# Kernel optimization log

Measured on AMD Instinct MI355X. Metric: run time of the kernel, lower is better.

Reference implementation:

```python
import jax, jax.numpy as jnp
import numpy as np

B, S, D, H = 4, 1024, 1024, 16
DK = D // H
EPS = 1e-6


def setup_inputs() -> dict:
    key = jax.random.key(0)
    ks = jax.random.split(key, 12)
    s = 1.0 / np.sqrt(D)
    inp = {
        "query": jax.random.normal(ks[0], (B, S, D), jnp.float32),
        "key": jax.random.normal(ks[1], (B, S, D), jnp.float32),
        "value": jax.random.normal(ks[2], (B, S, D), jnp.float32),
        "Wq": jax.random.normal(ks[3], (D, D), jnp.float32) * s,
        "bq": jnp.zeros((D,), jnp.float32),
        "Wk": jax.random.normal(ks[4], (D, D), jnp.float32) * s,
        "bk": jnp.zeros((D,), jnp.float32),
        "Wv": jax.random.normal(ks[5], (D, D), jnp.float32) * s,
        "bv": jnp.zeros((D,), jnp.float32),
        "Wo": jax.random.normal(ks[6], (D, D), jnp.float32) * s,
        "bo": jnp.zeros((D,), jnp.float32),
        "gamma": jnp.ones((D,), jnp.float32),
        "beta": jnp.zeros((D,), jnp.float32),
    }
    return inp


def reference(query, key, value, Wq, bq, Wk, bk, Wv, bv, Wo, bo, gamma, beta):
    residual = query
    # QKV projections, split into heads: [B,S,D] -> [B,H,S,DK]
    q = (query @ Wq + bq).reshape(B, S, H, DK).transpose(0, 2, 1, 3)
    k = (key @ Wk + bk).reshape(B, S, H, DK).transpose(0, 2, 1, 3)
    v = (value @ Wv + bv).reshape(B, S, H, DK).transpose(0, 2, 1, 3)
    # scaled dot-product attention (dropout is identity in eval mode)
    scores = jnp.einsum("bhqd,bhkd->bhqk", q, k) / jnp.sqrt(jnp.float32(DK))
    attn = jax.nn.softmax(scores, axis=-1)  # [B,H,S,S]
    x = jnp.einsum("bhqk,bhkd->bhqd", attn, v)
    x = x.transpose(0, 2, 1, 3).reshape(B, S, D)
    # residual + LayerNorm(eps=1e-6)
    x = x + residual
    mu = jnp.mean(x, axis=-1, keepdims=True)
    var = jnp.mean(jnp.square(x - mu), axis=-1, keepdims=True)
    x = (x - mu) * jax.lax.rsqrt(var + EPS) * gamma + beta
    out = x @ Wo + bo
    return (out, attn)
```

## Files before the change

### kernel.cpp

```cpp
#include <hip/hip_runtime.h>

typedef unsigned short u16;
typedef __attribute__((ext_vector_type(8))) short bf16x8;
typedef __attribute__((ext_vector_type(4))) float f32x4;

struct __align__(8) us4 { u16 x, y, z, w; };

#define B_  4
#define S_  1024
#define D_  1024
#define H_  16
#define DK_ 64

__device__ __forceinline__ u16 f2bf(float x) {
    union { float f; unsigned int u; } c; c.f = x;
    unsigned int r = (c.u + 0x7FFFu + ((c.u >> 16) & 1u)) >> 16;
    return (u16)r;
}

__device__ __forceinline__ void gload_lds16(const void* g, void* l) {
    __builtin_amdgcn_global_load_lds(
        (const __attribute__((address_space(1))) unsigned int*)g,
        (__attribute__((address_space(3))) unsigned int*)l, 16, 0, 0);
}

__global__ __launch_bounds__(256) void cvt_x(const float* __restrict__ q,
                                             const float* __restrict__ k,
                                             const float* __restrict__ v,
                                             u16* __restrict__ xq,
                                             u16* __restrict__ xk,
                                             u16* __restrict__ xv) {
    const float* src = (blockIdx.y == 0) ? q : (blockIdx.y == 1) ? k : v;
    u16* dst        = (blockIdx.y == 0) ? xq : (blockIdx.y == 1) ? xk : xv;
    int idx = (blockIdx.x * 256 + threadIdx.x) * 4;
    f32x4 f = *(const f32x4*)(src + idx);
    us4 o; o.x = f2bf(f[0]); o.y = f2bf(f[1]); o.z = f2bf(f[2]); o.w = f2bf(f[3]);
    *(us4*)(dst + idx) = o;
}

__global__ __launch_bounds__(256) void cvt_w(const float* __restrict__ w0, const float* __restrict__ w1,
                                             const float* __restrict__ w2, const float* __restrict__ w3,
                                             u16* __restrict__ t0, u16* __restrict__ t1,
                                             u16* __restrict__ t2, u16* __restrict__ t3) {
    __shared__ float t[64][65];
    const float* W = (blockIdx.z == 0) ? w0 : (blockIdx.z == 1) ? w1 : (blockIdx.z == 2) ? w2 : w3;
    u16* T        = (blockIdx.z == 0) ? t0 : (blockIdx.z == 1) ? t1 : (blockIdx.z == 2) ? t2 : t3;
    int k0 = blockIdx.x * 64, n0 = blockIdx.y * 64;
    int tid = threadIdx.x;
    int r4 = tid >> 6, c = tid & 63;
#pragma unroll
    for (int i = 0; i < 16; i++) {
        int r = i * 4 + r4;
        t[r][c] = W[(size_t)(k0 + r) * 1024 + n0 + c];
    }
    __syncthreads();
#pragma unroll
    for (int i = 0; i < 16; i++) {
        int r = i * 4 + r4;
        T[(size_t)(n0 + r) * 1024 + k0 + c] = f2bf(t[c][r]);
    }
}

__device__ __forceinline__ void gemm_core(const u16* __restrict__ X, const u16* __restrict__ WT,
                                          const float* __restrict__ bias, void* __restrict__ outp,
                                          int mode, float scale, int bm, int bn) {
    __shared__ u16 Al[128 * 32];
    __shared__ u16 Bl[128 * 32];
    int tid = threadIdx.x, l = tid & 63, w = tid >> 6;
    int lr = l & 15, lq = l >> 4;
    int wm = (w >> 1) * 64, wn = (w & 1) * 64;
    f32x4 acc[4][4] = {};
    for (int kk = 0; kk < 1024; kk += 32) {
        __syncthreads();
#pragma unroll
        for (int i = 0; i < 2; i++) {
            int flat = tid * 16 + i * 4096;
            int row = flat >> 6, kb = flat & 63;
            gload_lds16((const char*)X + ((size_t)(bm * 128 + row) * 2048 + (size_t)kk * 2 + kb),
                        (char*)Al + flat);
            gload_lds16((const char*)WT + ((size_t)(bn * 128 + row) * 2048 + (size_t)kk * 2 + kb),
                        (char*)Bl + flat);
        }
        asm volatile("s_waitcnt vmcnt(0)" ::: "memory");
        __syncthreads();
        bf16x8 af[4], bfr[4];
#pragma unroll
        for (int ms = 0; ms < 4; ms++)
            af[ms] = *(const bf16x8*)(Al + (wm + ms * 16 + lr) * 32 + lq * 8);
#pragma unroll
        for (int ns = 0; ns < 4; ns++)
            bfr[ns] = *(const bf16x8*)(Bl + (wn + ns * 16 + lr) * 32 + lq * 8);
#pragma unroll
        for (int ms = 0; ms < 4; ms++)
#pragma unroll
            for (int ns = 0; ns < 4; ns++)
                acc[ms][ns] = __builtin_amdgcn_mfma_f32_16x16x32_bf16(af[ms], bfr[ns], acc[ms][ns], 0, 0, 0);
    }
#pragma unroll
    for (int ns = 0; ns < 4; ns++) {
        int n = bn * 128 + wn + ns * 16 + lr;
        float bv_ = bias[n];
#pragma unroll
        for (int ms = 0; ms < 4; ms++) {
            int mbase = bm * 128 + wm + ms * 16 + lq * 4;
            if (mode == 0) {
                u16* o = (u16*)outp;
                int h = n >> 6, dk = n & 63;
#pragma unroll
                for (int r = 0; r < 4; r++) {
                    int m = mbase + r;
                    int b = m >> 10, s = m & 1023;
                    o[((size_t)(b * H_ + h) * 1024 + s) * 64 + dk] = f2bf((acc[ms][ns][r] + bv_) * scale);
                }
            } else if (mode == 1) {
                u16* o = (u16*)outp;
                int h = n >> 6, dk = n & 63;
                int b = mbase >> 10, s0 = mbase & 1023;
                us4 pk;
                pk.x = f2bf(acc[ms][ns][0] + bv_);
                pk.y = f2bf(acc[ms][ns][1] + bv_);
                pk.z = f2bf(acc[ms][ns][2] + bv_);
                pk.w = f2bf(acc[ms][ns][3] + bv_);
                *(us4*)(o + ((size_t)(b * H_ + h) * 64 + dk) * 1024 + s0) = pk;
            } else {
                float* o = (float*)outp;
#pragma unroll
                for (int r = 0; r < 4; r++) {
                    int m = mbase + r;
                    o[(size_t)m * 1024 + n] = acc[ms][ns][r] + bv_;
                }
            }
        }
    }
}

__global__ __launch_bounds__(256) void gemm_qkv(const u16* __restrict__ Xq, const u16* __restrict__ Xk,
                                                const u16* __restrict__ Xv,
                                                const u16* __restrict__ Wq, const u16* __restrict__ Wk,
                                                const u16* __restrict__ Wv,
                                                const float* __restrict__ bq, const float* __restrict__ bk,
                                                const float* __restrict__ bv,
                                                u16* __restrict__ Qh, u16* __restrict__ Kh,
                                                u16* __restrict__ VT) {
    int z = blockIdx.z;
    const u16* X = (z == 0) ? Xq : (z == 1) ? Xk : Xv;
    const u16* W = (z == 0) ? Wq : (z == 1) ? Wk : Wv;
    const float* bia = (z == 0) ? bq : (z == 1) ? bk : bv;
    void* out = (z == 0) ? (void*)Qh : (z == 1) ? (void*)Kh : (void*)VT;
    int mode = (z == 2) ? 1 : 0;
    float scale = (z == 0) ? 0.125f : 1.0f;
    gemm_core(X, W, bia, out, mode, scale, blockIdx.x, blockIdx.y);
}

__global__ __launch_bounds__(256) void gemm_out(const u16* __restrict__ X, const u16* __restrict__ WT,
                                                const float* __restrict__ bias, float* __restrict__ outp) {
    gemm_core(X, WT, bias, outp, 2, 1.0f, blockIdx.x, blockIdx.y);
}

__global__ __launch_bounds__(256) void attn_fused(const u16* __restrict__ Qh, const u16* __restrict__ Kh,
                                                  const u16* __restrict__ VT,
                                                  float* __restrict__ attn_out, float* __restrict__ x_out) {
    __shared__ u16 P_lds[4][4096];
    __shared__ float red[4][16][64];
    __shared__ float redm[4][16];
    __shared__ float reds[4][16];
    int tid = threadIdx.x, l = tid & 63, w = tid >> 6;
    int lr = l & 15, lq = l >> 4;
    int q0 = blockIdx.x * 16, bh = blockIdx.y;
    const u16* qp = Qh + (size_t)bh * 65536;
    const u16* kp = Kh + (size_t)bh * 65536;
    const u16* vp = VT + (size_t)bh * 65536;

    bf16x8 aq0 = *(const bf16x8*)(qp + (q0 + lr) * 64 + lq * 8);
    bf16x8 aq1 = *(const bf16x8*)(qp + (q0 + lr) * 64 + 32 + lq * 8);

    f32x4 sc[16];
#pragma unroll
    for (int n = 0; n < 16; n++) {
        int kb = w * 256 + n * 16;
        bf16x8 b0 = *(const bf16x8*)(kp + (size_t)(kb + lr) * 64 + lq * 8);
        bf16x8 b1 = *(const bf16x8*)(kp + (size_t)(kb + lr) * 64 + 32 + lq * 8);
        f32x4 a = {};
        a = __builtin_amdgcn_mfma_f32_16x16x32_bf16(aq0, b0, a, 0, 0, 0);
        a = __builtin_amdgcn_mfma_f32_16x16x32_bf16(aq1, b1, a, 0, 0, 0);
        sc[n] = a;
    }

#pragma unroll
    for (int r = 0; r < 4; r++) {
        float m = sc[0][r];
#pragma unroll
        for (int n = 1; n < 16; n++) m = fmaxf(m, sc[n][r]);
#pragma unroll
        for (int off = 1; off < 16; off <<= 1) m = fmaxf(m, __shfl_xor(m, off));
        if (lr == 0) redm[w][lq * 4 + r] = m;
    }
    __syncthreads();
    float inv[4];
#pragma unroll
    for (int r = 0; r < 4; r++) {
        int row = lq * 4 + r;
        float M = fmaxf(fmaxf(redm[0][row], redm[1][row]), fmaxf(redm[2][row], redm[3][row]));
        float s = 0.f;
#pragma unroll
        for (int n = 0; n < 16; n++) {
            float p = __expf(sc[n][r] - M);
            sc[n][r] = p;
            s += p;
        }
#pragma unroll
        for (int off = 1; off < 16; off <<= 1) s += __shfl_xor(s, off);
        if (lr == 0) reds[w][row] = s;
    }
    __syncthreads();
#pragma unroll
    for (int r = 0; r < 4; r++) {
        int row = lq * 4 + r;
        inv[r] = 1.0f / (reds[0][row] + reds[1][row] + reds[2][row] + reds[3][row]);
    }

    size_t abase = (size_t)bh * 1048576 + (size_t)q0 * 1024 + w * 256;
#pragma unroll
    for (int n = 0; n < 16; n++) {
#pragma unroll
        for (int r = 0; r < 4; r++) {
            float p = sc[n][r] * inv[r];
            attn_out[abase + (size_t)(lq * 4 + r) * 1024 + n * 16 + lr] = p;
            int row = lq * 4 + r, col = n * 16 + lr;
            P_lds[w][row * 256 + (col ^ ((row & 3) << 4))] = f2bf(p);
        }
    }
    __syncthreads();

    f32x4 pv[4] = {};
#pragma unroll
    for (int kk = 0; kk < 8; kk++) {
        int col = kk * 32 + lq * 8;
        bf16x8 ap = *(const bf16x8*)(&P_lds[w][lr * 256 + (col ^ ((lr & 3) << 4))]);
#pragma unroll
        for (int ns = 0; ns < 4; ns++) {
            bf16x8 bv_ = *(const bf16x8*)(vp + (size_t)(ns * 16 + lr) * 1024 + w * 256 + kk * 32 + lq * 8);
            pv[ns] = __builtin_amdgcn_mfma_f32_16x16x32_bf16(ap, bv_, pv[ns], 0, 0, 0);
        }
    }
#pragma unroll
    for (int ns = 0; ns < 4; ns++)
#pragma unroll
        for (int r = 0; r < 4; r++)
            red[w][lq * 4 + r][ns * 16 + lr] = pv[ns][r];
    __syncthreads();

    int qq = tid >> 4, dk = (tid & 15) * 4;
    f32x4 acc = *(const f32x4*)&red[0][qq][dk];
#pragma unroll
    for (int w2 = 1; w2 < 4; w2++) acc += *(const f32x4*)&red[w2][qq][dk];
    int b = bh >> 4, h = bh & 15;
    *(f32x4*)(x_out + ((size_t)(b * 1024 + q0 + qq)) * 1024 + h * 64 + dk) = acc;
}

__global__ __launch_bounds__(256) void ln_kernel(const float* __restrict__ x, const float* __restrict__ resid,
                                                 const float* __restrict__ gamma, const float* __restrict__ beta,
                                                 u16* __restrict__ out) {
    int row = blockIdx.x, tid = threadIdx.x;
    int l = tid & 63, w = tid >> 6;
    size_t base = (size_t)row * 1024 + tid * 4;
    f32x4 v = *(const f32x4*)(x + base);
    f32x4 rz = *(const f32x4*)(resid + base);
    v += rz;
    float s = v[0] + v[1] + v[2] + v[3];
    float s2 = v[0] * v[0] + v[1] * v[1] + v[2] * v[2] + v[3] * v[3];
#pragma unroll
    for (int off = 1; off < 64; off <<= 1) {
        s += __shfl_xor(s, off);
        s2 += __shfl_xor(s2, off);
    }
    __shared__ float as_[4], as2_[4];
    if (l == 0) { as_[w] = s; as2_[w] = s2; }
    __syncthreads();
    s = as_[0] + as_[1] + as_[2] + as_[3];
    s2 = as2_[0] + as2_[1] + as2_[2] + as2_[3];
    float mean = s * (1.f / 1024.f);
    float var = s2 * (1.f / 1024.f) - mean * mean;
    float rs = rsqrtf(var + 1e-6f);
    f32x4 g = *(const f32x4*)(gamma + tid * 4);
    f32x4 bt = *(const f32x4*)(beta + tid * 4);
    us4 o;
    o.x = f2bf((v[0] - mean) * rs * g[0] + bt[0]);
    o.y = f2bf((v[1] - mean) * rs * g[1] + bt[1]);
    o.z = f2bf((v[2] - mean) * rs * g[2] + bt[2]);
    o.w = f2bf((v[3] - mean) * rs * g[3] + bt[3]);
    *(us4*)(out + base) = o;
}

extern "C" void kernel_launch(void* const* d_in, const int* in_sizes, int n_in,
                              void* d_out, int out_size, void* d_ws, size_t ws_size,
                              hipStream_t stream) {
    const float* query = (const float*)d_in[0];
    const float* key   = (const float*)d_in[1];
    const float* value = (const float*)d_in[2];
    const float* Wq    = (const float*)d_in[3];
    const float* bq    = (const float*)d_in[4];
    const float* Wk    = (const float*)d_in[5];
    const float* bk    = (const float*)d_in[6];
    const float* Wv    = (const float*)d_in[7];
    const float* bv    = (const float*)d_in[8];
    const float* Wo    = (const float*)d_in[9];
    const float* bo    = (const float*)d_in[10];
    const float* gamma = (const float*)d_in[11];
    const float* beta  = (const float*)d_in[12];

    char* ws = (char*)d_ws;
    u16* XQ  = (u16*)(ws + 0);
    u16* XK  = (u16*)(ws + 8388608);
    u16* XV  = (u16*)(ws + 16777216);
    u16* WQT = (u16*)(ws + 25165824);
    u16* WKT = (u16*)(ws + 27262976);
    u16* WVT = (u16*)(ws + 29360128);
    u16* WOT = (u16*)(ws + 31457280);
    u16* Qh  = (u16*)(ws + 33554432);
    u16* Kh  = (u16*)(ws + 41943040);
    u16* VT  = (u16*)(ws + 50331648);
    float* PV = (float*)(ws + 0);
    u16* LN  = (u16*)(ws + 16777216);

    float* outp = (float*)d_out;
    float* attn = outp + 4194304;

    cvt_x<<<dim3(4096, 3), 256, 0, stream>>>(query, key, value, XQ, XK, XV);
    cvt_w<<<dim3(16, 16, 4), 256, 0, stream>>>(Wq, Wk, Wv, Wo, WQT, WKT, WVT, WOT);
    gemm_qkv<<<dim3(32, 8, 3), 256, 0, stream>>>(XQ, XK, XV, WQT, WKT, WVT, bq, bk, bv, Qh, Kh, VT);
    attn_fused<<<dim3(64, 64), 256, 0, stream>>>(Qh, Kh, VT, attn, PV);
    ln_kernel<<<4096, 256, 0, stream>>>(PV, query, gamma, beta, LN);
    gemm_out<<<dim3(32, 8), 256, 0, stream>>>(LN, WOT, bo, outp);
}
```

Before: 249.3 us.

## Deepen GEMM K-tile, narrow output GEMM tile, and remap attention blocks per XCD

```diff
diff --git a/kernel.cpp b/kernel.cpp
--- a/kernel.cpp
+++ b/kernel.cpp
@@ -61,49 +61,59 @@
     }
 }
 
+template <int BN, int MODE>
 __device__ __forceinline__ void gemm_core(const u16* __restrict__ X, const u16* __restrict__ WT,
                                           const float* __restrict__ bias, void* __restrict__ outp,
-                                          int mode, float scale, int bm, int bn) {
-    __shared__ u16 Al[128 * 32];
-    __shared__ u16 Bl[128 * 32];
+                                          float scale, int bm, int bn) {
+    constexpr int NS = BN / 32;
+    __shared__ u16 Al[128 * 64];
+    __shared__ u16 Bl[BN * 64];
     int tid = threadIdx.x, l = tid & 63, w = tid >> 6;
     int lr = l & 15, lq = l >> 4;
-    int wm = (w >> 1) * 64, wn = (w & 1) * 64;
-    f32x4 acc[4][4] = {};
-    for (int kk = 0; kk < 1024; kk += 32) {
+    int wm = (w >> 1) * 64, wn = (w & 1) * (BN / 2);
+    f32x4 acc[4][NS] = {};
+    for (int kk = 0; kk < 1024; kk += 64) {
         __syncthreads();
 #pragma unroll
-        for (int i = 0; i < 2; i++) {
+        for (int i = 0; i < 4; i++) {
             int flat = tid * 16 + i * 4096;
-            int row = flat >> 6, kb = flat & 63;
+            int row = flat >> 7, kb = flat & 127;
             gload_lds16((const char*)X + ((size_t)(bm * 128 + row) * 2048 + (size_t)kk * 2 + kb),
                         (char*)Al + flat);
-            gload_lds16((const char*)WT + ((size_t)(bn * 128 + row) * 2048 + (size_t)kk * 2 + kb),
+        }
+#pragma unroll
+        for (int i = 0; i < BN / 32; i++) {
+            int flat = tid * 16 + i * 4096;
+            int row = flat >> 7, kb = flat & 127;
+            gload_lds16((const char*)WT + ((size_t)(bn * BN + row) * 2048 + (size_t)kk * 2 + kb),
                         (char*)Bl + flat);
         }
         asm volatile("s_waitcnt vmcnt(0)" ::: "memory");
         __syncthreads();
-        bf16x8 af[4], bfr[4];
-#pragma unroll
-        for (int ms = 0; ms < 4; ms++)
-            af[ms] = *(const bf16x8*)(Al + (wm + ms * 16 + lr) * 32 + lq * 8);
-#pragma unroll
-        for (int ns = 0; ns < 4; ns++)
-            bfr[ns] = *(const bf16x8*)(Bl + (wn + ns * 16 + lr) * 32 + lq * 8);
-#pragma unroll
-        for (int ms = 0; ms < 4; ms++)
-#pragma unroll
-            for (int ns = 0; ns < 4; ns++)
-                acc[ms][ns] = __builtin_amdgcn_mfma_f32_16x16x32_bf16(af[ms], bfr[ns], acc[ms][ns], 0, 0, 0);
-    }
-#pragma unroll
-    for (int ns = 0; ns < 4; ns++) {
-        int n = bn * 128 + wn + ns * 16 + lr;
+#pragma unroll
+        for (int kkk = 0; kkk < 2; kkk++) {
+            bf16x8 af[4], bfr[NS];
+#pragma unroll
+            for (int ms = 0; ms < 4; ms++)
+                af[ms] = *(const bf16x8*)(Al + (wm + ms * 16 + lr) * 64 + kkk * 32 + lq * 8);
+#pragma unroll
+            for (int ns = 0; ns < NS; ns++)
+                bfr[ns] = *(const bf16x8*)(Bl + (wn + ns * 16 + lr) * 64 + kkk * 32 + lq * 8);
+#pragma unroll
+            for (int ms = 0; ms < 4; ms++)
+#pragma unroll
+                for (int ns = 0; ns < NS; ns++)
+                    acc[ms][ns] = __builtin_amdgcn_mfma_f32_16x16x32_bf16(af[ms], bfr[ns], acc[ms][ns], 0, 0, 0);
+        }
+    }
+#pragma unroll
+    for (int ns = 0; ns < NS; ns++) {
+        int n = bn * BN + wn + ns * 16 + lr;
         float bv_ = bias[n];
 #pragma unroll
         for (int ms = 0; ms < 4; ms++) {
             int mbase = bm * 128 + wm + ms * 16 + lq * 4;
-            if (mode == 0) {
+            if (MODE == 0) {
                 u16* o = (u16*)outp;
                 int h = n >> 6, dk = n & 63;
 #pragma unroll
@@ -112,7 +122,7 @@
                     int b = m >> 10, s = m & 1023;
                     o[((size_t)(b * H_ + h) * 1024 + s) * 64 + dk] = f2bf((acc[ms][ns][r] + bv_) * scale);
                 }
-            } else if (mode == 1) {
+            } else if (MODE == 1) {
                 u16* o = (u16*)outp;
                 int h = n >> 6, dk = n & 63;
                 int b = mbase >> 10, s0 = mbase & 1023;
@@ -146,15 +156,17 @@
     const u16* X = (z == 0) ? Xq : (z == 1) ? Xk : Xv;
     const u16* W = (z == 0) ? Wq : (z == 1) ? Wk : Wv;
     const float* bia = (z == 0) ? bq : (z == 1) ? bk : bv;
-    void* out = (z == 0) ? (void*)Qh : (z == 1) ? (void*)Kh : (void*)VT;
-    int mode = (z == 2) ? 1 : 0;
-    float scale = (z == 0) ? 0.125f : 1.0f;
-    gemm_core(X, W, bia, out, mode, scale, blockIdx.x, blockIdx.y);
+    if (z == 2)
+        gemm_core<128, 1>(X, W, bia, (void*)VT, 1.0f, blockIdx.x, blockIdx.y);
+    else if (z == 0)
+        gemm_core<128, 0>(X, W, bia, (void*)Qh, 0.125f, blockIdx.x, blockIdx.y);
+    else
+        gemm_core<128, 0>(X, W, bia, (void*)Kh, 1.0f, blockIdx.x, blockIdx.y);
 }
 
 __global__ __launch_bounds__(256) void gemm_out(const u16* __restrict__ X, const u16* __restrict__ WT,
                                                 const float* __restrict__ bias, float* __restrict__ outp) {
-    gemm_core(X, WT, bias, outp, 2, 1.0f, blockIdx.x, blockIdx.y);
+    gemm_core<64, 2>(X, WT, bias, outp, 1.0f, blockIdx.x, blockIdx.y);
 }
 
 __global__ __launch_bounds__(256) void attn_fused(const u16* __restrict__ Qh, const u16* __restrict__ Kh,
@@ -166,7 +178,11 @@
     __shared__ float reds[4][16];
     int tid = threadIdx.x, l = tid & 63, w = tid >> 6;
     int lr = l & 15, lq = l >> 4;
-    int q0 = blockIdx.x * 16, bh = blockIdx.y;
+    int wg = blockIdx.x;
+    int xcd = wg & 7;
+    int rest = wg >> 3;
+    int q0 = (rest & 63) * 16;
+    int bh = ((rest >> 6) << 3) | xcd;
     const u16* qp = Qh + (size_t)bh * 65536;
     const u16* kp = Kh + (size_t)bh * 65536;
     const u16* vp = VT + (size_t)bh * 65536;
@@ -329,7 +345,7 @@
     cvt_x<<<dim3(4096, 3), 256, 0, stream>>>(query, key, value, XQ, XK, XV);
     cvt_w<<<dim3(16, 16, 4), 256, 0, stream>>>(Wq, Wk, Wv, Wo, WQT, WKT, WVT, WOT);
     gemm_qkv<<<dim3(32, 8, 3), 256, 0, stream>>>(XQ, XK, XV, WQT, WKT, WVT, bq, bk, bv, Qh, Kh, VT);
-    attn_fused<<<dim3(64, 64), 256, 0, stream>>>(Qh, Kh, VT, attn, PV);
+    attn_fused<<<dim3(4096), 256, 0, stream>>>(Qh, Kh, VT, attn, PV);
     ln_kernel<<<4096, 256, 0, stream>>>(PV, query, gamma, beta, LN);
-    gemm_out<<<dim3(32, 8), 256, 0, stream>>>(LN, WOT, bo, outp);
-}
+    gemm_out<<<dim3(32, 16), 256, 0, stream>>>(LN, WOT, bo, outp);
+}
```

New measurement: 245.8 us. No clear change (-1.4%).
